# Optimization experiments

Hardware: AMD Instinct MI355X
Metric: run time of the kernel (lower is better)

Reference implementation:

```python
import jax, jax.numpy as jnp
import numpy as np

B, S, DIN, DOUT = 4, 2048, 4096, 4096

def setup_inputs() -> dict:
    key = jax.random.key(0)
    k1, k2, k3, k4 = jax.random.split(key, 4)
    x = jax.random.normal(k1, (B, S, DIN), dtype=jnp.float32)
    base_T = jax.random.normal(k2, (DIN, DOUT), dtype=jnp.float32) * 0.02
    # mask bit = 1 where (finetune - base) >= 0, else 0; sign matrix = 2*mask - 1
    mask_bits = jax.random.randint(k3, (DIN, DOUT), 0, 2, dtype=jnp.int32)
    # coeff = mean |diff| quantile scalar (learned); a small positive scalar
    coeff = jax.random.uniform(k4, (1,), dtype=jnp.float32) * 0.01
    return {"x": x, "base_T": base_T, "mask_bits": mask_bits, "coeff": coeff}

def reference(x, base_T, mask_bits, coeff):
    # binary_bmm over packed mask == matmul with {-1,+1} sign matrix
    signs = (2 * mask_bits - 1).astype(x.dtype)           # [DIN, DOUT] in {-1,+1}
    dense = jnp.einsum('bsi,io->bso', x, base_T)          # x @ base.T
    corr = jnp.einsum('bsi,io->bso', x, signs)            # binary correction
    return dense + coeff[0] * corr
```

## Files before the change

### kernel.cpp

```cpp
#include <hip/hip_runtime.h>
#include <hip/hip_bf16.h>
#include <stdint.h>

#define DIN   4096
#define DOUT  4096
#define MROWS 8192

typedef __bf16 bf16_t;
typedef __attribute__((ext_vector_type(8))) __bf16 bf16x8;
typedef __attribute__((ext_vector_type(4))) float   f32x4;

__device__ __forceinline__ unsigned short f2bf(float f) {
    union { float f; unsigned u; } v; v.f = f;
    unsigned r = v.u + 0x7FFFu + ((v.u >> 16) & 1u);
    return (unsigned short)(r >> 16);
}

__global__ __launch_bounds__(256)
void build_wt(const float* __restrict__ baseT,
              const int*   __restrict__ mask,
              const float* __restrict__ coeff,
              unsigned short* __restrict__ Wt) {
    __shared__ float tile[64][68];
    const float c = coeff[0];
    const int t  = threadIdx.x;
    const int n0 = blockIdx.x * 64;
    const int k0 = blockIdx.y * 64;

    const int kr = t >> 4;
    const int nv = (t & 15) * 4;
#pragma unroll
    for (int i = 0; i < 4; ++i) {
        const int kl = i * 16 + kr;
        const size_t idx = (size_t)(k0 + kl) * DOUT + n0 + nv;
        float4 b4 = *(const float4*)(baseT + idx);
        int4   m4 = *(const int4*)(mask + idx);
        float4 v;
        v.x = b4.x + c * (float)(2 * m4.x - 1);
        v.y = b4.y + c * (float)(2 * m4.y - 1);
        v.z = b4.z + c * (float)(2 * m4.z - 1);
        v.w = b4.w + c * (float)(2 * m4.w - 1);
        *(float4*)&tile[kl][nv] = v;
    }
    __syncthreads();

    const int nr = t >> 4;
    const int kv = (t & 15) * 4;
#pragma unroll
    for (int j = 0; j < 4; ++j) {
        const int nl = j * 16 + nr;
        ushort4 o;
        o.x = f2bf(tile[kv + 0][nl]);
        o.y = f2bf(tile[kv + 1][nl]);
        o.z = f2bf(tile[kv + 2][nl]);
        o.w = f2bf(tile[kv + 3][nl]);
        *(ushort4*)(Wt + (size_t)(n0 + nl) * DIN + k0 + kv) = o;
    }
}

__global__ __launch_bounds__(256)
void cvt_x(const float* __restrict__ x, unsigned short* __restrict__ xb) {
    const int i = blockIdx.x * 256 + threadIdx.x;
    const float4* xv = (const float4*)x;
    float4 a = xv[4 * i + 0];
    float4 b = xv[4 * i + 1];
    float4 c = xv[4 * i + 2];
    float4 d = xv[4 * i + 3];
    union { ushort4 s[2]; uint4 u; } p0, p1;
    p0.s[0] = make_ushort4(f2bf(a.x), f2bf(a.y), f2bf(a.z), f2bf(a.w));
    p0.s[1] = make_ushort4(f2bf(b.x), f2bf(b.y), f2bf(b.z), f2bf(b.w));
    p1.s[0] = make_ushort4(f2bf(c.x), f2bf(c.y), f2bf(c.z), f2bf(c.w));
    p1.s[1] = make_ushort4(f2bf(d.x), f2bf(d.y), f2bf(d.z), f2bf(d.w));
    uint4* ov = (uint4*)xb;
    ov[2 * i + 0] = p0.u;
    ov[2 * i + 1] = p1.u;
}

__global__ __launch_bounds__(256, 2)
void gemm_bt(const unsigned short* __restrict__ X,
             const unsigned short* __restrict__ Wt,
             float* __restrict__ out) {
    __shared__ __align__(16) bf16_t sA[128 * 64];
    __shared__ __align__(16) bf16_t sB[128 * 64];

    const int tid  = threadIdx.x;
    const int lane = tid & 63;
    const int wv   = tid >> 6;
    const int bm   = blockIdx.x & 63;
    const int bn   = blockIdx.x >> 6;
    const int wm   = wv >> 1;
    const int wn   = wv & 1;

    const int row0  = wv * 32 + (lane >> 3);
    const int kcol  = ((lane & 7) ^ (lane >> 3)) * 8;
    const unsigned short* gA = X  + (size_t)(bm * 128 + row0) * DIN + kcol;
    const unsigned short* gB = Wt + (size_t)(bn * 128 + row0) * DIN + kcol;
    bf16_t* lA = sA + wv * 2048;
    bf16_t* lB = sB + wv * 2048;

    const int arow  = wm * 64 + (lane & 15);
    const int brow  = wn * 64 + (lane & 15);
    const int koff0 = (((lane >> 4) + 0) ^ (lane & 7)) * 8;
    const int koff1 = (((lane >> 4) + 4) ^ (lane & 7)) * 8;

    f32x4 acc[4][4];
#pragma unroll
    for (int i = 0; i < 4; ++i)
#pragma unroll
        for (int j = 0; j < 4; ++j) acc[i][j] = (f32x4){0.f, 0.f, 0.f, 0.f};

    for (int kt = 0; kt < DIN / 64; ++kt) {
#pragma unroll
        for (int i = 0; i < 4; ++i)
            __builtin_amdgcn_global_load_lds(
                (const __attribute__((address_space(1))) void*)(gA + (size_t)i * 8 * DIN),
                (__attribute__((address_space(3))) void*)(lA + i * 512), 16, 0, 0);
#pragma unroll
        for (int i = 0; i < 4; ++i)
            __builtin_amdgcn_global_load_lds(
                (const __attribute__((address_space(1))) void*)(gB + (size_t)i * 8 * DIN),
                (__attribute__((address_space(3))) void*)(lB + i * 512), 16, 0, 0);
        gA += 64; gB += 64;
        __syncthreads();

#pragma unroll
        for (int ks = 0; ks < 2; ++ks) {
            const int ko = ks ? koff1 : koff0;
            bf16x8 af[4], bfr[4];
#pragma unroll
            for (int mi = 0; mi < 4; ++mi)
                af[mi] = *(const bf16x8*)&sA[(arow + mi * 16) * 64 + ko];
#pragma unroll
            for (int ni = 0; ni < 4; ++ni)
                bfr[ni] = *(const bf16x8*)&sB[(brow + ni * 16) * 64 + ko];
#pragma unroll
            for (int mi = 0; mi < 4; ++mi)
#pragma unroll
                for (int ni = 0; ni < 4; ++ni)
                    acc[mi][ni] = __builtin_amdgcn_mfma_f32_16x16x32_bf16(
                        af[mi], bfr[ni], acc[mi][ni], 0, 0, 0);
        }
        __syncthreads();
    }

    const int crow0 = bm * 128 + wm * 64 + (lane >> 4) * 4;
    const int ccol0 = bn * 128 + wn * 64 + (lane & 15);
#pragma unroll
    for (int mi = 0; mi < 4; ++mi)
#pragma unroll
        for (int ni = 0; ni < 4; ++ni)
#pragma unroll
            for (int r = 0; r < 4; ++r)
                out[(size_t)(crow0 + mi * 16 + r) * DOUT + (ccol0 + ni * 16)] =
                    acc[mi][ni][r];
}

extern "C" void kernel_launch(void* const* d_in, const int* in_sizes, int n_in,
                              void* d_out, int out_size, void* d_ws, size_t ws_size,
                              hipStream_t stream) {
    const float* x     = (const float*)d_in[0];
    const float* baseT = (const float*)d_in[1];
    const int*   mask  = (const int*)d_in[2];
    const float* coeff = (const float*)d_in[3];

    unsigned short* Wt = (unsigned short*)d_ws;
    unsigned short* Xb = (unsigned short*)((char*)d_ws + (size_t)DIN * DOUT * 2);
    float* out = (float*)d_out;

    build_wt<<<dim3(DOUT / 64, DIN / 64), 256, 0, stream>>>(baseT, mask, coeff, Wt);

    cvt_x<<<(MROWS * DIN / 16) / 256, 256, 0, stream>>>(x, Xb);

    gemm_bt<<<64 * 32, 256, 0, stream>>>(Xb, Wt, out);
}
```

Measured before the change: 559.0 us.

## Rewrite GEMM as 256x256 tile, 8-wave double-buffered ping-pong pipeline

The bf16 GEMM kernel moves from 128x128 tiles with 4 waves and a single LDS buffer to 256x256 tiles with 8 waves and double-buffered LDS. Global-to-LDS loads for the next K slice are interleaved with MFMA phases, gated by explicit waitcnt, barriers, sched_barriers and setprio. Blocks are remapped across XCDs for locality. The aim is to hide load latency and raise reuse per LDS byte, at the cost of 128KB LDS per block and more register pressure, with some risk to correctness from the hand-tuned waitcnt counts.

```diff
diff --git a/kernel.cpp b/kernel.cpp
--- a/kernel.cpp
+++ b/kernel.cpp
@@ -76,77 +76,130 @@
     ov[2 * i + 1] = p1.u;
 }
 
-__global__ __launch_bounds__(256, 2)
+#define AS1 __attribute__((address_space(1)))
+#define AS3 __attribute__((address_space(3)))
+#define GLD16(src, dst) \
+    __builtin_amdgcn_global_load_lds((const AS1 void*)(src), (AS3 void*)(dst), 16, 0, 0)
+#define SB __builtin_amdgcn_sched_barrier(0)
+
+#define PH_HEAD do { SB; __builtin_amdgcn_s_barrier(); \
+    asm volatile("s_waitcnt lgkmcnt(0)" ::: "memory"); SB; \
+    __builtin_amdgcn_s_setprio(1); } while (0)
+#define PH_TAIL do { __builtin_amdgcn_s_setprio(0); SB; \
+    __builtin_amdgcn_s_barrier(); SB; } while (0)
+#define PH_TAIL_VM do { __builtin_amdgcn_s_setprio(0); SB; \
+    asm volatile("s_waitcnt vmcnt(4)" ::: "memory"); \
+    __builtin_amdgcn_s_barrier(); SB; } while (0)
+
+#define STG_A(b, h, kb) do { \
+    GLD16(gA + (size_t)((h) * 128 + 0) * DIN + (kb), &sA[b][(h) * 8192 + wv * 1024 + 0]);   \
+    GLD16(gA + (size_t)((h) * 128 + 8) * DIN + (kb), &sA[b][(h) * 8192 + wv * 1024 + 512]); \
+} while (0)
+#define STG_B(b, h, kb) do { \
+    GLD16(gB + (size_t)((h) * 128 + 0) * DIN + (kb), &sB[b][(h) * 8192 + wv * 1024 + 0]);   \
+    GLD16(gB + (size_t)((h) * 128 + 8) * DIN + (kb), &sB[b][(h) * 8192 + wv * 1024 + 512]); \
+} while (0)
+
+#define RD_AF0(b) do { _Pragma("unroll") \
+    for (int mi = 0; mi < 4; ++mi) { \
+        af0[mi][0] = *(const bf16x8*)&sA[b][aRow + mi * 1024 + ko0]; \
+        af0[mi][1] = *(const bf16x8*)&sA[b][aRow + mi * 1024 + ko1]; } } while (0)
+#define RD_AF1(b) do { _Pragma("unroll") \
+    for (int mi = 0; mi < 4; ++mi) { \
+        af1[mi][0] = *(const bf16x8*)&sA[b][aRow + (4 + mi) * 1024 + ko0]; \
+        af1[mi][1] = *(const bf16x8*)&sA[b][aRow + (4 + mi) * 1024 + ko1]; } } while (0)
+#define RD_BF0(b) do { _Pragma("unroll") \
+    for (int ni = 0; ni < 2; ++ni) { \
+        bf0[ni][0] = *(const bf16x8*)&sB[b][bRow + ni * 1024 + ko0]; \
+        bf0[ni][1] = *(const bf16x8*)&sB[b][bRow + ni * 1024 + ko1]; } } while (0)
+#define RD_BF1(b) do { _Pragma("unroll") \
+    for (int ni = 0; ni < 2; ++ni) { \
+        bf1[ni][0] = *(const bf16x8*)&sB[b][bRow + (2 + ni) * 1024 + ko0]; \
+        bf1[ni][1] = *(const bf16x8*)&sB[b][bRow + (2 + ni) * 1024 + ko1]; } } while (0)
+
+#define MM(afr, mbase, bfr, nbase) do { _Pragma("unroll") \
+    for (int mi = 0; mi < 4; ++mi) { _Pragma("unroll") \
+        for (int ni = 0; ni < 2; ++ni) { \
+            acc[(mbase) + mi][(nbase) + ni] = __builtin_amdgcn_mfma_f32_16x16x32_bf16( \
+                afr[mi][0], bfr[ni][0], acc[(mbase) + mi][(nbase) + ni], 0, 0, 0); \
+            acc[(mbase) + mi][(nbase) + ni] = __builtin_amdgcn_mfma_f32_16x16x32_bf16( \
+                afr[mi][1], bfr[ni][1], acc[(mbase) + mi][(nbase) + ni], 0, 0, 0); } } } while (0)
+
+__global__ __launch_bounds__(512, 2)
 void gemm_bt(const unsigned short* __restrict__ X,
              const unsigned short* __restrict__ Wt,
              float* __restrict__ out) {
-    __shared__ __align__(16) bf16_t sA[128 * 64];
-    __shared__ __align__(16) bf16_t sB[128 * 64];
+    __shared__ __align__(16) bf16_t sA[2][256 * 64];
+    __shared__ __align__(16) bf16_t sB[2][256 * 64];
 
     const int tid  = threadIdx.x;
     const int lane = tid & 63;
     const int wv   = tid >> 6;
-    const int bm   = blockIdx.x & 63;
-    const int bn   = blockIdx.x >> 6;
-    const int wm   = wv >> 1;
-    const int wn   = wv & 1;
-
-    const int row0  = wv * 32 + (lane >> 3);
-    const int kcol  = ((lane & 7) ^ (lane >> 3)) * 8;
-    const unsigned short* gA = X  + (size_t)(bm * 128 + row0) * DIN + kcol;
-    const unsigned short* gB = Wt + (size_t)(bn * 128 + row0) * DIN + kcol;
-    bf16_t* lA = sA + wv * 2048;
-    bf16_t* lB = sB + wv * 2048;
-
-    const int arow  = wm * 64 + (lane & 15);
-    const int brow  = wn * 64 + (lane & 15);
-    const int koff0 = (((lane >> 4) + 0) ^ (lane & 7)) * 8;
-    const int koff1 = (((lane >> 4) + 4) ^ (lane & 7)) * 8;
-
-    f32x4 acc[4][4];
-#pragma unroll
-    for (int i = 0; i < 4; ++i)
+    const int wm   = wv >> 2;
+    const int wn   = wv & 3;
+
+    const int bid = blockIdx.x;
+    const int wg  = (bid & 7) * 64 + (bid >> 3);
+    const int bm  = wg & 31;
+    const int bn  = wg >> 5;
+
+    const int r8   = lane >> 3;
+    const int kcol = ((lane & 7) ^ r8) * 8;
+    const unsigned short* gA = X  + (size_t)(bm * 256 + wv * 16 + r8) * DIN + kcol;
+    const unsigned short* gB = Wt + (size_t)(bn * 256 + wv * 16 + r8) * DIN + kcol;
+
+    const int l15  = lane & 15;
+    const int l7   = lane & 7;
+    const int aRow = (wm * 128 + l15) * 64;
+    const int bRow = (wn * 64 + l15) * 64;
+    const int ko0  = (((lane >> 4) + 0) ^ l7) * 8;
+    const int ko1  = (((lane >> 4) + 4) ^ l7) * 8;
+
+    bf16x8 af0[4][2], af1[4][2], bf0[2][2], bf1[2][2];
+    f32x4 acc[8][4];
+#pragma unroll
+    for (int i = 0; i < 8; ++i)
 #pragma unroll
         for (int j = 0; j < 4; ++j) acc[i][j] = (f32x4){0.f, 0.f, 0.f, 0.f};
 
-    for (int kt = 0; kt < DIN / 64; ++kt) {
-#pragma unroll
-        for (int i = 0; i < 4; ++i)
-            __builtin_amdgcn_global_load_lds(
-                (const __attribute__((address_space(1))) void*)(gA + (size_t)i * 8 * DIN),
-                (__attribute__((address_space(3))) void*)(lA + i * 512), 16, 0, 0);
-#pragma unroll
-        for (int i = 0; i < 4; ++i)
-            __builtin_amdgcn_global_load_lds(
-                (const __attribute__((address_space(1))) void*)(gB + (size_t)i * 8 * DIN),
-                (__attribute__((address_space(3))) void*)(lB + i * 512), 16, 0, 0);
-        gA += 64; gB += 64;
-        __syncthreads();
-
-#pragma unroll
-        for (int ks = 0; ks < 2; ++ks) {
-            const int ko = ks ? koff1 : koff0;
-            bf16x8 af[4], bfr[4];
-#pragma unroll
-            for (int mi = 0; mi < 4; ++mi)
-                af[mi] = *(const bf16x8*)&sA[(arow + mi * 16) * 64 + ko];
-#pragma unroll
-            for (int ni = 0; ni < 4; ++ni)
-                bfr[ni] = *(const bf16x8*)&sB[(brow + ni * 16) * 64 + ko];
-#pragma unroll
-            for (int mi = 0; mi < 4; ++mi)
-#pragma unroll
-                for (int ni = 0; ni < 4; ++ni)
-                    acc[mi][ni] = __builtin_amdgcn_mfma_f32_16x16x32_bf16(
-                        af[mi], bfr[ni], acc[mi][ni], 0, 0, 0);
-        }
-        __syncthreads();
+    STG_A(0, 0, 0); STG_A(0, 1, 0);
+    STG_B(0, 0, 0); STG_B(0, 1, 0);
+    STG_A(1, 0, 64); STG_A(1, 1, 64);
+    asm volatile("s_waitcnt vmcnt(4)" ::: "memory");
+    __builtin_amdgcn_s_barrier();
+    SB;
+
+#pragma unroll 1
+    for (int it = 0; it < DIN / 128; ++it) {
+        const int kB1 = it * 128 + 64;
+        const int k0  = (it * 128 + 128) & (DIN - 1);
+        const int kA1 = (it * 128 + 192) & (DIN - 1);
+
+        RD_AF0(0); RD_BF0(0); STG_B(1, 0, kB1);
+        asm volatile("s_waitcnt lgkmcnt(8)" ::: "memory");
+        PH_HEAD; MM(af0, 0, bf0, 0); PH_TAIL;
+        RD_AF1(0); STG_B(1, 1, kB1);
+        PH_HEAD; MM(af1, 4, bf0, 0); PH_TAIL;
+        RD_BF1(0); STG_A(0, 0, k0);
+        PH_HEAD; MM(af1, 4, bf1, 2); PH_TAIL;
+        STG_A(0, 1, k0);
+        PH_HEAD; MM(af0, 0, bf1, 2); PH_TAIL_VM;
+
+        RD_AF0(1); RD_BF0(1); STG_B(0, 0, k0);
+        asm volatile("s_waitcnt lgkmcnt(8)" ::: "memory");
+        PH_HEAD; MM(af0, 0, bf0, 0); PH_TAIL;
+        RD_AF1(1); STG_B(0, 1, k0);
+        PH_HEAD; MM(af1, 4, bf0, 0); PH_TAIL;
+        RD_BF1(1); STG_A(1, 0, kA1);
+        PH_HEAD; MM(af1, 4, bf1, 2); PH_TAIL;
+        STG_A(1, 1, kA1);
+        PH_HEAD; MM(af0, 0, bf1, 2); PH_TAIL_VM;
     }
 
-    const int crow0 = bm * 128 + wm * 64 + (lane >> 4) * 4;
-    const int ccol0 = bn * 128 + wn * 64 + (lane & 15);
-#pragma unroll
-    for (int mi = 0; mi < 4; ++mi)
+    const int crow0 = bm * 256 + wm * 128 + (lane >> 4) * 4;
+    const int ccol0 = bn * 256 + wn * 64 + l15;
+#pragma unroll
+    for (int mi = 0; mi < 8; ++mi)
 #pragma unroll
         for (int ni = 0; ni < 4; ++ni)
 #pragma unroll
@@ -171,5 +224,5 @@
 
     cvt_x<<<(MROWS * DIN / 16) / 256, 256, 0, stream>>>(x, Xb);
 
-    gemm_bt<<<64 * 32, 256, 0, stream>>>(Xb, Wt, out);
-}
+    gemm_bt<<<(MROWS / 256) * (DOUT / 256), 512, 0, stream>>>(Xb, Wt, out);
+}
```

Result: slower. 601.4 us (+7.6%).
